# Performance work log

Hardware: AMD Instinct MI355X
Metric: run time of the kernel (lower is better)

Reference implementation:

```python
import jax, jax.numpy as jnp
import numpy as np

ALPHA = 0.2  # LeakyReLU negative slope
NEG = -9e15


def gat_layer(h, adj, W, a):
    # Faithful to the torch GAT: e_ij = leakyrelu(a^T [Wh_i || Wh_j])
    # = leakyrelu(a_src . Wh_i + a_dst . Wh_j); avoids the NxNx2F materialization.
    Wh = h @ W                              # [N, F]
    Fo = W.shape[1]
    a_src, a_dst = a[:Fo, 0], a[Fo:, 0]
    e = jax.nn.leaky_relu(
        (Wh @ a_src)[:, None] + (Wh @ a_dst)[None, :], negative_slope=ALPHA
    )                                        # [N, N]
    e = jnp.where(adj > 0, e, NEG)
    att = jax.nn.softmax(e, axis=1)          # dropout p=0 (eval)
    return jax.nn.elu(att @ Wh)


def gru_cell(x, h, W_ih, W_hh, b_ih, b_hh):
    # PyTorch GRUCell semantics.
    gi = x @ W_ih.T + b_ih                   # [N, 3F]
    gh = h @ W_hh.T + b_hh
    i_r, i_z, i_n = jnp.split(gi, 3, axis=1)
    h_r, h_z, h_n = jnp.split(gh, 3, axis=1)
    r = jax.nn.sigmoid(i_r + h_r)
    z = jax.nn.sigmoid(i_z + h_z)
    n = jnp.tanh(i_n + r * h_n)
    return (1.0 - z) * n + z * h


def setup_inputs() -> dict:
    key = jax.random.key(0)
    ks = jax.random.split(key, 10)
    N, nfeat, nhid, nout = 8192, 256, 128, 128
    x = jax.random.normal(ks[0], (N, nfeat), dtype=jnp.float32)
    # sparse random binary adjacency (~32 avg degree) + self loops
    adj = (jax.random.uniform(ks[1], (N, N)) < 0.004).astype(jnp.float32)
    adj = jnp.maximum(adj, jnp.eye(N, dtype=jnp.float32))
    h_prev = jnp.zeros((N, nout), dtype=jnp.float32)

    def xavier(k, shape, gain=1.414):
        fan_in, fan_out = shape[0], shape[1]
        b = gain * np.sqrt(6.0 / (fan_in + fan_out))
        return jax.random.uniform(k, shape, jnp.float32, -b, b)

    W1 = xavier(ks[2], (nfeat, nhid))
    a1 = xavier(ks[3], (2 * nhid, 1))
    W2 = xavier(ks[4], (nhid, nout))
    a2 = xavier(ks[5], (2 * nout, 1))
    s = 1.0 / np.sqrt(nout)
    W_ih = jax.random.uniform(ks[6], (3 * nout, nout), jnp.float32, -s, s)
    W_hh = jax.random.uniform(ks[7], (3 * nout, nout), jnp.float32, -s, s)
    b_ih = jax.random.uniform(ks[8], (3 * nout,), jnp.float32, -s, s)
    b_hh = jax.random.uniform(ks[9], (3 * nout,), jnp.float32, -s, s)
    return {"x": x, "adj": adj, "h_prev": h_prev, "W1": W1, "a1": a1,
            "W2": W2, "a2": a2, "W_ih": W_ih, "W_hh": W_hh,
            "b_ih": b_ih, "b_hh": b_hh}


def reference(x, adj, h_prev, W1, a1, W2, a2, W_ih, W_hh, b_ih, b_hh):
    x1 = gat_layer(x, adj, W1, a1)
    h_spat = gat_layer(x1, adj, W2, a2)
    return gru_cell(h_spat, h_prev, W_ih, W_hh, b_ih, b_hh)
```

## Files before the change

kernel.cpp:

```cpp
#include <hip/hip_runtime.h>
#include <math.h>

#define N_NODES 8192
#define CAP 128
#define LRELU_ALPHA 0.2f

typedef float v4f __attribute__((ext_vector_type(4)));

template <int K>
__device__ __forceinline__ void gemm_srcdst_body(
    int r0, int t, const float* __restrict__ A, const float* __restrict__ W,
    const float* __restrict__ a, float* __restrict__ Wh, float* __restrict__ src,
    float* __restrict__ dst, float* As, float (*red)[4][2]) {
  int c = t & 127, half = t >> 7;
  const float4* Ab4 = (const float4*)(A + (size_t)r0 * K);
  float4* As4 = (float4*)As;
#pragma unroll
  for (int l = t; l < 8 * K / 4; l += 256) As4[l] = Ab4[l];
  __syncthreads();
  float acc[4] = {0.f, 0.f, 0.f, 0.f};
  const float* Asl = As + (half * 4) * K;
#pragma unroll 4
  for (int k = 0; k < K; k++) {
    float wv = W[k * 128 + c];
#pragma unroll
    for (int r = 0; r < 4; r++) acc[r] += Asl[r * K + k] * wv;
  }
  float as = a[c], ad = a[128 + c];
  int wv_id = t >> 6, lane = t & 63;
#pragma unroll
  for (int r = 0; r < 4; r++) {
    int row = half * 4 + r;
    Wh[(size_t)(r0 + row) * 128 + c] = acc[r];
    float s = acc[r] * as, d = acc[r] * ad;
#pragma unroll
    for (int off = 32; off; off >>= 1) {
      s += __shfl_xor(s, off);
      d += __shfl_xor(d, off);
    }
    if (lane == 0) { red[wv_id][r][0] = s; red[wv_id][r][1] = d; }
  }
  __syncthreads();
  if (t < 8) {
    int wa = (t < 4) ? 0 : 2, rr = t & 3;
    src[r0 + t] = red[wa][rr][0] + red[wa + 1][rr][0];
    dst[r0 + t] = red[wa][rr][1] + red[wa + 1][rr][1];
  }
}

#define ADJ_B 8192
#define G1_B 1024
#define TR_B 64
__global__ void phase1_kernel(const float* __restrict__ adj, int* __restrict__ idx,
                              int* __restrict__ counts, const float* __restrict__ x,
                              const float* __restrict__ W1, const float* __restrict__ a1,
                              float* __restrict__ Wh1, float* __restrict__ src1,
                              float* __restrict__ dst1, const float* __restrict__ Wi,
                              const float* __restrict__ Whm, float* __restrict__ WiT,
                              float* __restrict__ WhT) {
  __shared__ float As[8 * 256];
  __shared__ float red[4][4][2];
  __shared__ int cnt;
  int t = threadIdx.x;
  int bid = blockIdx.x;
  if (bid < ADJ_B) {
    if (t == 0) cnt = 0;
    __syncthreads();
    const v4f* row = (const v4f*)(adj + (size_t)bid * N_NODES);
    int* outp = idx + (size_t)bid * CAP;
#pragma unroll 2
    for (int b = t; b < N_NODES / 4; b += 256) {
      v4f v = __builtin_nontemporal_load(row + b);
      int n = (v.x > 0.f) + (v.y > 0.f) + (v.z > 0.f) + (v.w > 0.f);
      if (n) {
        int p = atomicAdd(&cnt, n);
        int j0 = b * 4;
        if (v.x > 0.f) { if (p < CAP) outp[p] = j0;     p++; }
        if (v.y > 0.f) { if (p < CAP) outp[p] = j0 + 1; p++; }
        if (v.z > 0.f) { if (p < CAP) outp[p] = j0 + 2; p++; }
        if (v.w > 0.f) { if (p < CAP) outp[p] = j0 + 3; p++; }
      }
    }
    __syncthreads();
    if (t == 0) counts[bid] = cnt > CAP ? CAP : cnt;
  } else if (bid < ADJ_B + G1_B) {
    gemm_srcdst_body<256>((bid - ADJ_B) * 8, t, x, W1, a1, Wh1, src1, dst1, As, red);
  } else {
    int gid = (bid - ADJ_B - G1_B) * 256 + t;
    for (int n = gid; n < 384 * 128; n += TR_B * 256) {
      int r = n >> 7, c = n & 127;
      WiT[c * 384 + r] = Wi[n];
      WhT[c * 384 + r] = Whm[n];
    }
  }
}

__global__ void gemm_srcdst2_kernel(const float* __restrict__ A, const float* __restrict__ W,
                                    const float* __restrict__ a, float* __restrict__ Wh,
                                    float* __restrict__ src, float* __restrict__ dst) {
  __shared__ float As[8 * 128];
  __shared__ float red[4][4][2];
  gemm_srcdst_body<128>(blockIdx.x * 8, threadIdx.x, A, W, a, Wh, src, dst, As, red);
}

__global__ void gat_aggregate_kernel(const float* __restrict__ Wh, const float* __restrict__ src,
                                     const float* __restrict__ dst, const int* __restrict__ idx,
                                     const int* __restrict__ counts, float* __restrict__ outp) {
  __shared__ float w[CAP];
  __shared__ int jn[CAP];
  __shared__ float redm[2];
  __shared__ float reds[2];
  int i = blockIdx.x, t = threadIdx.x;
  int cnt = counts[i];
  float si = src[i];
  float v = -1e30f;
  if (t < cnt) {
    int j = idx[(size_t)i * CAP + t];
    jn[t] = j;
    float e = si + dst[j];
    v = e > 0.f ? e : LRELU_ALPHA * e;
  }
  float m = v;
#pragma unroll
  for (int off = 32; off > 0; off >>= 1) m = fmaxf(m, __shfl_xor(m, off));
  if ((t & 63) == 0) redm[t >> 6] = m;
  __syncthreads();
  float M = fmaxf(redm[0], redm[1]);
  float ex = 0.f;
  if (t < cnt) {
    ex = expf(v - M);
    w[t] = ex;
  }
  float s = ex;
#pragma unroll
  for (int off = 32; off > 0; off >>= 1) s += __shfl_xor(s, off);
  if ((t & 63) == 0) reds[t >> 6] = s;
  __syncthreads();
  float inv = 1.f / (reds[0] + reds[1]);
  float acc = 0.f;
  int k = 0;
  for (; k + 4 <= cnt; k += 4) {
    float w0 = w[k], w1 = w[k + 1], w2 = w[k + 2], w3 = w[k + 3];
    int j0 = jn[k], j1 = jn[k + 1], j2 = jn[k + 2], j3 = jn[k + 3];
    acc += w0 * Wh[(size_t)j0 * 128 + t] + w1 * Wh[(size_t)j1 * 128 + t] +
           w2 * Wh[(size_t)j2 * 128 + t] + w3 * Wh[(size_t)j3 * 128 + t];
  }
  for (; k < cnt; k++) acc += w[k] * Wh[(size_t)jn[k] * 128 + t];
  acc *= inv;
  outp[(size_t)i * 128 + t] = acc > 0.f ? acc : expf(acc) - 1.f;
}

__global__ void gru_kernel(const float* __restrict__ x, const float* __restrict__ h,
                           const float* __restrict__ WiT, const float* __restrict__ WhT,
                           const float* __restrict__ b_ih, const float* __restrict__ b_hh,
                           float* __restrict__ outp) {
  __shared__ float xs[8 * 128];
  __shared__ float hs[8 * 128];
  int t = threadIdx.x, c = t & 127, half = t >> 7;
  int r0 = blockIdx.x * 8;
  {
    const float4* xb = (const float4*)(x + (size_t)r0 * 128);
    const float4* hb = (const float4*)(h + (size_t)r0 * 128);
    ((float4*)xs)[t] = xb[t];
    ((float4*)hs)[t] = hb[t];
  }
  __syncthreads();
  const float* xsl = xs + half * 4 * 128;
  const float* hsl = hs + half * 4 * 128;
  float rg[4], zg[4];
  {
    float ai[4] = {0.f}, ah[4] = {0.f};
#pragma unroll 4
    for (int k = 0; k < 128; k++) {
      float wi = WiT[k * 384 + c];
      float wh = WhT[k * 384 + c];
#pragma unroll
      for (int r = 0; r < 4; r++) {
        ai[r] += xsl[r * 128 + k] * wi;
        ah[r] += hsl[r * 128 + k] * wh;
      }
    }
    float bi = b_ih[c], bh = b_hh[c];
#pragma unroll
    for (int r = 0; r < 4; r++) rg[r] = 1.f / (1.f + expf(-(ai[r] + bi + ah[r] + bh)));
  }
  {
    float ai[4] = {0.f}, ah[4] = {0.f};
#pragma unroll 4
    for (int k = 0; k < 128; k++) {
      float wi = WiT[k * 384 + 128 + c];
      float wh = WhT[k * 384 + 128 + c];
#pragma unroll
      for (int r = 0; r < 4; r++) {
        ai[r] += xsl[r * 128 + k] * wi;
        ah[r] += hsl[r * 128 + k] * wh;
      }
    }
    float bi = b_ih[128 + c], bh = b_hh[128 + c];
#pragma unroll
    for (int r = 0; r < 4; r++) zg[r] = 1.f / (1.f + expf(-(ai[r] + bi + ah[r] + bh)));
  }
  {
    float ai[4] = {0.f}, ah[4] = {0.f};
#pragma unroll 4
    for (int k = 0; k < 128; k++) {
      float wi = WiT[k * 384 + 256 + c];
      float wh = WhT[k * 384 + 256 + c];
#pragma unroll
      for (int r = 0; r < 4; r++) {
        ai[r] += xsl[r * 128 + k] * wi;
        ah[r] += hsl[r * 128 + k] * wh;
      }
    }
    float bi = b_ih[256 + c], bh = b_hh[256 + c];
#pragma unroll
    for (int r = 0; r < 4; r++) {
      float n = tanhf(ai[r] + bi + rg[r] * (ah[r] + bh));
      float o = (1.f - zg[r]) * n + zg[r] * hsl[r * 128 + c];
      outp[(size_t)(r0 + half * 4 + r) * 128 + c] = o;
    }
  }
}

extern "C" void kernel_launch(void* const* d_in, const int* in_sizes, int n_in,
                              void* d_out, int out_size, void* d_ws, size_t ws_size,
                              hipStream_t stream) {
  const float* x     = (const float*)d_in[0];
  const float* adj   = (const float*)d_in[1];
  const float* hprev = (const float*)d_in[2];
  const float* W1    = (const float*)d_in[3];
  const float* a1    = (const float*)d_in[4];
  const float* W2    = (const float*)d_in[5];
  const float* a2    = (const float*)d_in[6];
  const float* W_ih  = (const float*)d_in[7];
  const float* W_hh  = (const float*)d_in[8];
  const float* b_ih  = (const float*)d_in[9];
  const float* b_hh  = (const float*)d_in[10];
  float* outp = (float*)d_out;

  char* p = (char*)d_ws;
  float* Wh1    = (float*)p; p += (size_t)N_NODES * 128 * 4;
  float* Wh2    = (float*)p; p += (size_t)N_NODES * 128 * 4;
  float* x1     = (float*)p; p += (size_t)N_NODES * 128 * 4;
  float* h_spat = (float*)p; p += (size_t)N_NODES * 128 * 4;
  float* src1   = (float*)p; p += (size_t)N_NODES * 4;
  float* dst1   = (float*)p; p += (size_t)N_NODES * 4;
  float* src2   = (float*)p; p += (size_t)N_NODES * 4;
  float* dst2   = (float*)p; p += (size_t)N_NODES * 4;
  float* WiT    = (float*)p; p += (size_t)384 * 128 * 4;
  float* WhT    = (float*)p; p += (size_t)384 * 128 * 4;
  int*   counts = (int*)p;   p += (size_t)N_NODES * 4;
  int*   idxbuf = (int*)p;   p += (size_t)N_NODES * CAP * 4;

  phase1_kernel<<<ADJ_B + G1_B + TR_B, 256, 0, stream>>>(
      adj, idxbuf, counts, x, W1, a1, Wh1, src1, dst1, W_ih, W_hh, WiT, WhT);
  gat_aggregate_kernel<<<N_NODES, 128, 0, stream>>>(Wh1, src1, dst1, idxbuf, counts, x1);
  gemm_srcdst2_kernel<<<N_NODES / 8, 256, 0, stream>>>(x1, W2, a2, Wh2, src2, dst2);
  gat_aggregate_kernel<<<N_NODES, 128, 0, stream>>>(Wh2, src2, dst2, idxbuf, counts, h_spat);
  gru_kernel<<<N_NODES / 8, 256, 0, stream>>>(h_spat, hprev, WiT, WhT, b_ih, b_hh, outp);
}
```

Measured before the change: 490.6 us.

## Fuse adjacency scan into first GAT aggregation, split neighbor sum across two halves

Moves the dense adjacency row scan out of the phase-1 kernel and fuses it with the first-layer attention aggregation, so neighbor indices stay in shared memory and no separate idx readback is needed. The whole 8192-float row is loaded upfront per thread with 8 nontemporal vector loads to raise memory-level parallelism. Aggregation now uses 256 threads, with two halves each summing alternate neighbors and combining through shared memory. A GEMM unroll factor and launch bounds are also changed. The scan now has to wait for the first GEMM, so it can no longer overlap with it.

Result: slower. 512.9 us (+4.6%).

```diff
diff --git a/kernel.cpp b/kernel.cpp
--- a/kernel.cpp
+++ b/kernel.cpp
@@ -20,7 +20,7 @@
   __syncthreads();
   float acc[4] = {0.f, 0.f, 0.f, 0.f};
   const float* Asl = As + (half * 4) * K;
-#pragma unroll 4
+#pragma unroll 8
   for (int k = 0; k < K; k++) {
     float wv = W[k * 128 + c];
 #pragma unroll
@@ -48,46 +48,19 @@
   }
 }
 
-#define ADJ_B 8192
-#define G1_B 1024
 #define TR_B 64
-__global__ void phase1_kernel(const float* __restrict__ adj, int* __restrict__ idx,
-                              int* __restrict__ counts, const float* __restrict__ x,
-                              const float* __restrict__ W1, const float* __restrict__ a1,
-                              float* __restrict__ Wh1, float* __restrict__ src1,
-                              float* __restrict__ dst1, const float* __restrict__ Wi,
-                              const float* __restrict__ Whm, float* __restrict__ WiT,
-                              float* __restrict__ WhT) {
+__global__ __launch_bounds__(256) void gemm1_kernel(
+    const float* __restrict__ x, const float* __restrict__ W1, const float* __restrict__ a1,
+    float* __restrict__ Wh1, float* __restrict__ src1, float* __restrict__ dst1,
+    const float* __restrict__ Wi, const float* __restrict__ Whm, float* __restrict__ WiT,
+    float* __restrict__ WhT) {
   __shared__ float As[8 * 256];
   __shared__ float red[4][4][2];
-  __shared__ int cnt;
-  int t = threadIdx.x;
-  int bid = blockIdx.x;
-  if (bid < ADJ_B) {
-    if (t == 0) cnt = 0;
-    __syncthreads();
-    const v4f* row = (const v4f*)(adj + (size_t)bid * N_NODES);
-    int* outp = idx + (size_t)bid * CAP;
-#pragma unroll 2
-    for (int b = t; b < N_NODES / 4; b += 256) {
-      v4f v = __builtin_nontemporal_load(row + b);
-      int n = (v.x > 0.f) + (v.y > 0.f) + (v.z > 0.f) + (v.w > 0.f);
-      if (n) {
-        int p = atomicAdd(&cnt, n);
-        int j0 = b * 4;
-        if (v.x > 0.f) { if (p < CAP) outp[p] = j0;     p++; }
-        if (v.y > 0.f) { if (p < CAP) outp[p] = j0 + 1; p++; }
-        if (v.z > 0.f) { if (p < CAP) outp[p] = j0 + 2; p++; }
-        if (v.w > 0.f) { if (p < CAP) outp[p] = j0 + 3; p++; }
-      }
-    }
-    __syncthreads();
-    if (t == 0) counts[bid] = cnt > CAP ? CAP : cnt;
-  } else if (bid < ADJ_B + G1_B) {
-    gemm_srcdst_body<256>((bid - ADJ_B) * 8, t, x, W1, a1, Wh1, src1, dst1, As, red);
+  int t = threadIdx.x, bid = blockIdx.x;
+  if (bid < 1024) {
+    gemm_srcdst_body<256>(bid * 8, t, x, W1, a1, Wh1, src1, dst1, As, red);
   } else {
-    int gid = (bid - ADJ_B - G1_B) * 256 + t;
-    for (int n = gid; n < 384 * 128; n += TR_B * 256) {
+    for (int n = (bid - 1024) * 256 + t; n < 384 * 128; n += TR_B * 256) {
       int r = n >> 7, c = n & 127;
       WiT[c * 384 + r] = Wi[n];
       WhT[c * 384 + r] = Whm[n];
@@ -95,65 +68,139 @@
   }
 }
 
-__global__ void gemm_srcdst2_kernel(const float* __restrict__ A, const float* __restrict__ W,
-                                    const float* __restrict__ a, float* __restrict__ Wh,
-                                    float* __restrict__ src, float* __restrict__ dst) {
+__global__ __launch_bounds__(256) void scan_agg_kernel(
+    const float* __restrict__ adj, const float* __restrict__ Wh, const float* __restrict__ src,
+    const float* __restrict__ dst, int* __restrict__ idx, int* __restrict__ counts,
+    float* __restrict__ outp) {
+  __shared__ int jn[CAP];
+  __shared__ float w[CAP];
+  __shared__ float redm[4];
+  __shared__ float reds[4];
+  __shared__ float accs[128];
+  __shared__ int cnt;
+  int i = blockIdx.x, t = threadIdx.x, lane = t & 63, wv = t >> 6;
+  if (t == 0) cnt = 0;
+  __syncthreads();
+  const v4f* row = (const v4f*)(adj + (size_t)i * N_NODES);
+  v4f v[8];
+#pragma unroll
+  for (int u = 0; u < 8; u++) v[u] = __builtin_nontemporal_load(row + t + 256 * u);
+#pragma unroll
+  for (int u = 0; u < 8; u++) {
+    int n = (v[u].x > 0.f) + (v[u].y > 0.f) + (v[u].z > 0.f) + (v[u].w > 0.f);
+    if (n) {
+      int p = atomicAdd(&cnt, n);
+      int j0 = (t + 256 * u) * 4;
+      if (v[u].x > 0.f) { if (p < CAP) jn[p] = j0;     p++; }
+      if (v[u].y > 0.f) { if (p < CAP) jn[p] = j0 + 1; p++; }
+      if (v[u].z > 0.f) { if (p < CAP) jn[p] = j0 + 2; p++; }
+      if (v[u].w > 0.f) { if (p < CAP) jn[p] = j0 + 3; p++; }
+    }
+  }
+  __syncthreads();
+  int c = cnt > CAP ? CAP : cnt;
+  if (t < c) idx[(size_t)i * CAP + t] = jn[t];
+  if (t == 0) counts[i] = c;
+  float si = src[i];
+  float e = -1e30f;
+  if (t < c) {
+    float x = si + dst[jn[t]];
+    e = x > 0.f ? x : LRELU_ALPHA * x;
+  }
+  float m = e;
+#pragma unroll
+  for (int off = 32; off; off >>= 1) m = fmaxf(m, __shfl_xor(m, off));
+  if (lane == 0) redm[wv] = m;
+  __syncthreads();
+  float M = fmaxf(fmaxf(redm[0], redm[1]), fmaxf(redm[2], redm[3]));
+  float ex = 0.f;
+  if (t < c) {
+    ex = expf(e - M);
+    w[t] = ex;
+  }
+  float s = ex;
+#pragma unroll
+  for (int off = 32; off; off >>= 1) s += __shfl_xor(s, off);
+  if (lane == 0) reds[wv] = s;
+  __syncthreads();
+  float inv = 1.f / (reds[0] + reds[1] + reds[2] + reds[3]);
+  int col = t & 127, half = t >> 7;
+  float acc = 0.f;
+  int k = half;
+  for (; k + 2 < c; k += 4) {
+    acc += w[k] * Wh[(size_t)jn[k] * 128 + col] + w[k + 2] * Wh[(size_t)jn[k + 2] * 128 + col];
+  }
+  for (; k < c; k += 2) acc += w[k] * Wh[(size_t)jn[k] * 128 + col];
+  if (half == 0) accs[col] = acc;
+  __syncthreads();
+  if (half == 1) {
+    float a = (accs[col] + acc) * inv;
+    outp[(size_t)i * 128 + col] = a > 0.f ? a : expf(a) - 1.f;
+  }
+}
+
+__global__ __launch_bounds__(256) void agg2_kernel(
+    const float* __restrict__ Wh, const float* __restrict__ src, const float* __restrict__ dst,
+    const int* __restrict__ idx, const int* __restrict__ counts, float* __restrict__ outp) {
+  __shared__ int jn[CAP];
+  __shared__ float w[CAP];
+  __shared__ float redm[4];
+  __shared__ float reds[4];
+  __shared__ float accs[128];
+  int i = blockIdx.x, t = threadIdx.x, lane = t & 63, wv = t >> 6;
+  int c = counts[i];
+  float si = src[i];
+  float e = -1e30f;
+  if (t < c) {
+    int j = idx[(size_t)i * CAP + t];
+    jn[t] = j;
+    float x = si + dst[j];
+    e = x > 0.f ? x : LRELU_ALPHA * x;
+  }
+  float m = e;
+#pragma unroll
+  for (int off = 32; off; off >>= 1) m = fmaxf(m, __shfl_xor(m, off));
+  if (lane == 0) redm[wv] = m;
+  __syncthreads();
+  float M = fmaxf(fmaxf(redm[0], redm[1]), fmaxf(redm[2], redm[3]));
+  float ex = 0.f;
+  if (t < c) {
+    ex = expf(e - M);
+    w[t] = ex;
+  }
+  float s = ex;
+#pragma unroll
+  for (int off = 32; off; off >>= 1) s += __shfl_xor(s, off);
+  if (lane == 0) reds[wv] = s;
+  __syncthreads();
+  float inv = 1.f / (reds[0] + reds[1] + reds[2] + reds[3]);
+  int col = t & 127, half = t >> 7;
+  float acc = 0.f;
+  int k = half;
+  for (; k + 2 < c; k += 4) {
+    acc += w[k] * Wh[(size_t)jn[k] * 128 + col] + w[k + 2] * Wh[(size_t)jn[k + 2] * 128 + col];
+  }
+  for (; k < c; k += 2) acc += w[k] * Wh[(size_t)jn[k] * 128 + col];
+  if (half == 0) accs[col] = acc;
+  __syncthreads();
+  if (half == 1) {
+    float a = (accs[col] + acc) * inv;
+    outp[(size_t)i * 128 + col] = a > 0.f ? a : expf(a) - 1.f;
+  }
+}
+
+__global__ __launch_bounds__(256) void gemm_srcdst2_kernel(
+    const float* __restrict__ A, const float* __restrict__ W, const float* __restrict__ a,
+    float* __restrict__ Wh, float* __restrict__ src, float* __restrict__ dst) {
   __shared__ float As[8 * 128];
   __shared__ float red[4][4][2];
   gemm_srcdst_body<128>(blockIdx.x * 8, threadIdx.x, A, W, a, Wh, src, dst, As, red);
 }
 
-__global__ void gat_aggregate_kernel(const float* __restrict__ Wh, const float* __restrict__ src,
-                                     const float* __restrict__ dst, const int* __restrict__ idx,
-                                     const int* __restrict__ counts, float* __restrict__ outp) {
-  __shared__ float w[CAP];
-  __shared__ int jn[CAP];
-  __shared__ float redm[2];
-  __shared__ float reds[2];
-  int i = blockIdx.x, t = threadIdx.x;
-  int cnt = counts[i];
-  float si = src[i];
-  float v = -1e30f;
-  if (t < cnt) {
-    int j = idx[(size_t)i * CAP + t];
-    jn[t] = j;
-    float e = si + dst[j];
-    v = e > 0.f ? e : LRELU_ALPHA * e;
-  }
-  float m = v;
-#pragma unroll
-  for (int off = 32; off > 0; off >>= 1) m = fmaxf(m, __shfl_xor(m, off));
-  if ((t & 63) == 0) redm[t >> 6] = m;
-  __syncthreads();
-  float M = fmaxf(redm[0], redm[1]);
-  float ex = 0.f;
-  if (t < cnt) {
-    ex = expf(v - M);
-    w[t] = ex;
-  }
-  float s = ex;
-#pragma unroll
-  for (int off = 32; off > 0; off >>= 1) s += __shfl_xor(s, off);
-  if ((t & 63) == 0) reds[t >> 6] = s;
-  __syncthreads();
-  float inv = 1.f / (reds[0] + reds[1]);
-  float acc = 0.f;
-  int k = 0;
-  for (; k + 4 <= cnt; k += 4) {
-    float w0 = w[k], w1 = w[k + 1], w2 = w[k + 2], w3 = w[k + 3];
-    int j0 = jn[k], j1 = jn[k + 1], j2 = jn[k + 2], j3 = jn[k + 3];
-    acc += w0 * Wh[(size_t)j0 * 128 + t] + w1 * Wh[(size_t)j1 * 128 + t] +
-           w2 * Wh[(size_t)j2 * 128 + t] + w3 * Wh[(size_t)j3 * 128 + t];
-  }
-  for (; k < cnt; k++) acc += w[k] * Wh[(size_t)jn[k] * 128 + t];
-  acc *= inv;
-  outp[(size_t)i * 128 + t] = acc > 0.f ? acc : expf(acc) - 1.f;
-}
-
-__global__ void gru_kernel(const float* __restrict__ x, const float* __restrict__ h,
-                           const float* __restrict__ WiT, const float* __restrict__ WhT,
-                           const float* __restrict__ b_ih, const float* __restrict__ b_hh,
-                           float* __restrict__ outp) {
+__global__ __launch_bounds__(256) void gru_kernel(
+    const float* __restrict__ x, const float* __restrict__ h, const float* __restrict__ WiT,
+    const float* __restrict__ WhT, const float* __restrict__ b_ih,
+    const float* __restrict__ b_hh, float* __restrict__ outp) {
   __shared__ float xs[8 * 128];
   __shared__ float hs[8 * 128];
   int t = threadIdx.x, c = t & 127, half = t >> 7;
@@ -252,10 +299,9 @@
   int*   counts = (int*)p;   p += (size_t)N_NODES * 4;
   int*   idxbuf = (int*)p;   p += (size_t)N_NODES * CAP * 4;
 
-  phase1_kernel<<<ADJ_B + G1_B + TR_B, 256, 0, stream>>>(
-      adj, idxbuf, counts, x, W1, a1, Wh1, src1, dst1, W_ih, W_hh, WiT, WhT);
-  gat_aggregate_kernel<<<N_NODES, 128, 0, stream>>>(Wh1, src1, dst1, idxbuf, counts, x1);
+  gemm1_kernel<<<1024 + TR_B, 256, 0, stream>>>(x, W1, a1, Wh1, src1, dst1, W_ih, W_hh, WiT, WhT);
+  scan_agg_kernel<<<N_NODES, 256, 0, stream>>>(adj, Wh1, src1, dst1, idxbuf, counts, x1);
   gemm_srcdst2_kernel<<<N_NODES / 8, 256, 0, stream>>>(x1, W2, a2, Wh2, src2, dst2);
-  gat_aggregate_kernel<<<N_NODES, 128, 0, stream>>>(Wh2, src2, dst2, idxbuf, counts, h_spat);
+  agg2_kernel<<<N_NODES, 256, 0, stream>>>(Wh2, src2, dst2, idxbuf, counts, h_spat);
   gru_kernel<<<N_NODES / 8, 256, 0, stream>>>(h_spat, hprev, WiT, WhT, b_ih, b_hh, outp);
 }
```
